# Performance work log

Hardware: AMD Instinct MI355X
Metric: run time of the kernel (lower is better)

## Reference

```python
import jax, jax.numpy as jnp
import numpy as np

N_FIELDS = 26
VOCAB = 100000
EMBED = 16
BATCH = 16384
K = 16
N = N_FIELDS * EMBED  # 416


def setup_inputs() -> dict:
    key = jax.random.key(0)
    k1, k2, k3, k4, k5 = jax.random.split(key, 5)
    X = jax.random.randint(k1, (BATCH, N_FIELDS), 0, VOCAB, dtype=jnp.int64)
    tables = jax.random.normal(k2, (N_FIELDS, VOCAB, EMBED), dtype=jnp.float32) * 0.01
    W = jax.random.normal(k3, (N, 1), dtype=jnp.float32) * 0.05
    b = jax.random.normal(k4, (1,), dtype=jnp.float32)
    v = jax.random.normal(k5, (N, K), dtype=jnp.float32) * 0.05
    return {"X": X, "tables": tables, "W": W, "b": b, "v": v}


def reference(X, tables, W, b, v):
    # per-field gather: tables[f, X[:, f]] -> [B, F, E]
    emb = jax.vmap(lambda t, idx: t[idx], in_axes=(0, 1), out_axes=1)(tables, X)
    all_emb = emb.reshape(emb.shape[0], -1)  # [B, n] concat over fields
    linear_part = all_emb @ W + b  # [B, 1]
    xv = all_emb @ v               # [B, k]
    square_of_sum = xv * xv
    sum_of_square = (all_emb * all_emb) @ (v * v)
    interaction = 0.5 * jnp.sum(square_of_sum - sum_of_square, axis=-1, keepdims=True)
    return jax.nn.sigmoid(linear_part + interaction)
```

## Files before the change

### kernel.cpp

```cpp
#include <hip/hip_runtime.h>
#include <math.h>

#define NF 26
#define VOCAB 100000
#define EMB 16
#define BATCH 16384
#define KD 16
#define NTOT (NF * EMB)
#define NP 420

__global__ __launch_bounds__(256, 4) void fm_kernel(
    const int* __restrict__ X, const float* __restrict__ tables,
    const float* __restrict__ W, const float* __restrict__ bptr,
    const float* __restrict__ v, float* __restrict__ out) {
    __shared__ float vT[KD][NP];
    __shared__ float2 wvs[NTOT];

    const int tid = threadIdx.x;

    for (int t = tid; t < NTOT * KD; t += 256) {
        int n = t >> 4, kk = t & 15;
        vT[kk][n] = v[t];
    }
    for (int n = tid; n < NTOT; n += 256) {
        const float* vr = v + n * KD;
        float s = 0.f;
#pragma unroll
        for (int k2 = 0; k2 < KD; ++k2) s = fmaf(vr[k2], vr[k2], s);
        wvs[n] = make_float2(W[n], s);
    }
    __syncthreads();

    const int g = tid >> 4;
    const int k = tid & 15;
    const int row = blockIdx.x * 16 + g;

    int idx[NF];
    {
        const int2* xr = (const int2*)(X + row * NF);
#pragma unroll
        for (int i = 0; i < NF / 2; ++i) {
            int2 t2 = xr[i];
            idx[2 * i] = t2.x;
            idx[2 * i + 1] = t2.y;
        }
    }

    float xv0 = 0.f, xv1 = 0.f;
    float lin = 0.f, sos = 0.f;

    float4 A0, A1, A2, A3, B0, B1, B2, B3;
    float ekA, ekB;
    {
        const float* er = tables + (size_t)idx[0] * EMB;
        const float4* e4 = (const float4*)er;
        A0 = e4[0]; A1 = e4[1]; A2 = e4[2]; A3 = e4[3];
        ekA = er[k];
    }

#pragma unroll 2
    for (int f = 0; f < NF; ++f) {
        if (f + 1 < NF) {
            const float* er =
                tables + ((size_t)(f + 1) * VOCAB + (size_t)idx[f + 1]) * EMB;
            const float4* e4 = (const float4*)er;
            B0 = e4[0]; B1 = e4[1]; B2 = e4[2]; B3 = e4[3];
            ekB = er[k];
        }

        const int nb = f * EMB;
        const float4* vr = (const float4*)&vT[k][nb];
        float4 v0 = vr[0], v1 = vr[1], v2 = vr[2], v3 = vr[3];

        xv0 = fmaf(A0.x, v0.x, xv0);
        xv0 = fmaf(A0.y, v0.y, xv0);
        xv0 = fmaf(A0.z, v0.z, xv0);
        xv0 = fmaf(A0.w, v0.w, xv0);
        xv0 = fmaf(A1.x, v1.x, xv0);
        xv0 = fmaf(A1.y, v1.y, xv0);
        xv0 = fmaf(A1.z, v1.z, xv0);
        xv0 = fmaf(A1.w, v1.w, xv0);
        xv1 = fmaf(A2.x, v2.x, xv1);
        xv1 = fmaf(A2.y, v2.y, xv1);
        xv1 = fmaf(A2.z, v2.z, xv1);
        xv1 = fmaf(A2.w, v2.w, xv1);
        xv1 = fmaf(A3.x, v3.x, xv1);
        xv1 = fmaf(A3.y, v3.y, xv1);
        xv1 = fmaf(A3.z, v3.z, xv1);
        xv1 = fmaf(A3.w, v3.w, xv1);

        float2 w2 = wvs[nb + k];
        lin = fmaf(ekA, w2.x, lin);
        sos = fmaf(ekA * ekA, w2.y, sos);

        A0 = B0; A1 = B1; A2 = B2; A3 = B3; ekA = ekB;
    }

    const float xv = xv0 + xv1;
    float p = lin + 0.5f * (xv * xv - sos);
    p += __shfl_xor(p, 1, 16);
    p += __shfl_xor(p, 2, 16);
    p += __shfl_xor(p, 4, 16);
    p += __shfl_xor(p, 8, 16);

    if (k == 0) {
        const float z = p + bptr[0];
        out[row] = 1.0f / (1.0f + __expf(-z));
    }
}

extern "C" void kernel_launch(void* const* d_in, const int* in_sizes, int n_in,
                              void* d_out, int out_size, void* d_ws,
                              size_t ws_size, hipStream_t stream) {
    const int* X = (const int*)d_in[0];
    const float* tables = (const float*)d_in[1];
    const float* W = (const float*)d_in[2];
    const float* b = (const float*)d_in[3];
    const float* v = (const float*)d_in[4];
    float* out = (float*)d_out;

    fm_kernel<<<BATCH / 16, 256, 0, stream>>>(X, tables, W, b, v, out);
}
```

Before: 227.7 us.

## Split work by embedding element per lane and shuffle-reduce all K partials

Each of the 16 lanes for a row now loads only its own embedding element per field (one coalesced 64-byte row per field across the lane group), issued for all 26 fields up front, instead of every lane loading the full 16-float row plus one element. Each lane accumulates partial xv for all 16 factors, and a butterfly shuffle reduction across the 16 lanes combines them. The v layout in shared memory changes to row-major with a padded stride of 20. The aim is to cut redundant gather traffic and expose more independent loads, at the cost of 64 extra shuffles and more registers. Offsets are computed in 32-bit unsigned arithmetic, which fits the table size.

```diff
diff --git a/kernel.cpp b/kernel.cpp
--- a/kernel.cpp
+++ b/kernel.cpp
@@ -7,32 +7,32 @@
 #define BATCH 16384
 #define KD 16
 #define NTOT (NF * EMB)
-#define NP 420
+#define VSTRIDE 20
 
 __global__ __launch_bounds__(256, 4) void fm_kernel(
     const int* __restrict__ X, const float* __restrict__ tables,
     const float* __restrict__ W, const float* __restrict__ bptr,
     const float* __restrict__ v, float* __restrict__ out) {
-    __shared__ float vT[KD][NP];
+    __shared__ float vL[NTOT * VSTRIDE];
     __shared__ float2 wvs[NTOT];
 
     const int tid = threadIdx.x;
 
     for (int t = tid; t < NTOT * KD; t += 256) {
-        int n = t >> 4, kk = t & 15;
-        vT[kk][n] = v[t];
+        int n = t >> 4, k = t & 15;
+        vL[n * VSTRIDE + k] = v[t];
     }
     for (int n = tid; n < NTOT; n += 256) {
         const float* vr = v + n * KD;
         float s = 0.f;
 #pragma unroll
-        for (int k2 = 0; k2 < KD; ++k2) s = fmaf(vr[k2], vr[k2], s);
+        for (int k = 0; k < KD; ++k) s = fmaf(vr[k], vr[k], s);
         wvs[n] = make_float2(W[n], s);
     }
     __syncthreads();
 
     const int g = tid >> 4;
-    const int k = tid & 15;
+    const int j = tid & 15;
     const int row = blockIdx.x * 16 + g;
 
     int idx[NF];
@@ -46,65 +46,63 @@
         }
     }
 
-    float xv0 = 0.f, xv1 = 0.f;
+    float e[NF];
+#pragma unroll
+    for (int f = 0; f < NF; ++f) {
+        unsigned off =
+            (unsigned)(f * VOCAB + idx[f]) * (unsigned)(EMB * 4) + (j << 2);
+        e[f] = *(const float*)((const char*)tables + off);
+    }
+
+    float xv[KD];
+#pragma unroll
+    for (int k = 0; k < KD; ++k) xv[k] = 0.f;
     float lin = 0.f, sos = 0.f;
 
-    float4 A0, A1, A2, A3, B0, B1, B2, B3;
-    float ekA, ekB;
-    {
-        const float* er = tables + (size_t)idx[0] * EMB;
-        const float4* e4 = (const float4*)er;
-        A0 = e4[0]; A1 = e4[1]; A2 = e4[2]; A3 = e4[3];
-        ekA = er[k];
+#pragma unroll
+    for (int f = 0; f < NF; ++f) {
+        const int n = f * EMB + j;
+        const float4* vr = (const float4*)&vL[n * VSTRIDE];
+        float4 v0 = vr[0], v1 = vr[1], v2 = vr[2], v3 = vr[3];
+        const float ef = e[f];
+        xv[0] = fmaf(ef, v0.x, xv[0]);
+        xv[1] = fmaf(ef, v0.y, xv[1]);
+        xv[2] = fmaf(ef, v0.z, xv[2]);
+        xv[3] = fmaf(ef, v0.w, xv[3]);
+        xv[4] = fmaf(ef, v1.x, xv[4]);
+        xv[5] = fmaf(ef, v1.y, xv[5]);
+        xv[6] = fmaf(ef, v1.z, xv[6]);
+        xv[7] = fmaf(ef, v1.w, xv[7]);
+        xv[8] = fmaf(ef, v2.x, xv[8]);
+        xv[9] = fmaf(ef, v2.y, xv[9]);
+        xv[10] = fmaf(ef, v2.z, xv[10]);
+        xv[11] = fmaf(ef, v2.w, xv[11]);
+        xv[12] = fmaf(ef, v3.x, xv[12]);
+        xv[13] = fmaf(ef, v3.y, xv[13]);
+        xv[14] = fmaf(ef, v3.z, xv[14]);
+        xv[15] = fmaf(ef, v3.w, xv[15]);
+
+        float2 w2 = wvs[n];
+        lin = fmaf(ef, w2.x, lin);
+        sos = fmaf(ef * ef, w2.y, sos);
     }
 
-#pragma unroll 2
-    for (int f = 0; f < NF; ++f) {
-        if (f + 1 < NF) {
-            const float* er =
-                tables + ((size_t)(f + 1) * VOCAB + (size_t)idx[f + 1]) * EMB;
-            const float4* e4 = (const float4*)er;
-            B0 = e4[0]; B1 = e4[1]; B2 = e4[2]; B3 = e4[3];
-            ekB = er[k];
-        }
-
-        const int nb = f * EMB;
-        const float4* vr = (const float4*)&vT[k][nb];
-        float4 v0 = vr[0], v1 = vr[1], v2 = vr[2], v3 = vr[3];
-
-        xv0 = fmaf(A0.x, v0.x, xv0);
-        xv0 = fmaf(A0.y, v0.y, xv0);
-        xv0 = fmaf(A0.z, v0.z, xv0);
-        xv0 = fmaf(A0.w, v0.w, xv0);
-        xv0 = fmaf(A1.x, v1.x, xv0);
-        xv0 = fmaf(A1.y, v1.y, xv0);
-        xv0 = fmaf(A1.z, v1.z, xv0);
-        xv0 = fmaf(A1.w, v1.w, xv0);
-        xv1 = fmaf(A2.x, v2.x, xv1);
-        xv1 = fmaf(A2.y, v2.y, xv1);
-        xv1 = fmaf(A2.z, v2.z, xv1);
-        xv1 = fmaf(A2.w, v2.w, xv1);
-        xv1 = fmaf(A3.x, v3.x, xv1);
-        xv1 = fmaf(A3.y, v3.y, xv1);
-        xv1 = fmaf(A3.z, v3.z, xv1);
-        xv1 = fmaf(A3.w, v3.w, xv1);
-
-        float2 w2 = wvs[nb + k];
-        lin = fmaf(ekA, w2.x, lin);
-        sos = fmaf(ekA * ekA, w2.y, sos);
-
-        A0 = B0; A1 = B1; A2 = B2; A3 = B3; ekA = ekB;
+#pragma unroll
+    for (int m = 1; m < 16; m <<= 1) {
+#pragma unroll
+        for (int k = 0; k < KD; ++k) xv[k] += __shfl_xor(xv[k], m, 16);
     }
 
-    const float xv = xv0 + xv1;
-    float p = lin + 0.5f * (xv * xv - sos);
-    p += __shfl_xor(p, 1, 16);
-    p += __shfl_xor(p, 2, 16);
-    p += __shfl_xor(p, 4, 16);
-    p += __shfl_xor(p, 8, 16);
+    float ss = 0.f;
+#pragma unroll
+    for (int k = 0; k < KD; ++k) ss = fmaf(xv[k], xv[k], ss);
 
-    if (k == 0) {
-        const float z = p + bptr[0];
+    float t = fmaf(-0.5f, sos, lin);
+#pragma unroll
+    for (int m = 1; m < 16; m <<= 1) t += __shfl_xor(t, m, 16);
+
+    if (j == 0) {
+        const float z = t + 0.5f * ss + bptr[0];
         out[row] = 1.0f / (1.0f + __expf(-z));
     }
 }
```

Measured after the change: 220.0 us. 1.03x faster.
